# Kernel optimization log

Measured on AMD Instinct MI355X. Metric: run time of the kernel, lower is better.

Reference implementation:

```python
import jax, jax.numpy as jnp
import numpy as np

TEMPERATURE = 8.0  # sqrt(d_k=64)

def setup_inputs() -> dict:
    key = jax.random.key(0)
    kq, kk, kv, km1, km2 = jax.random.split(key, 5)
    B, Lq, Lk, D = 128, 512, 512, 64
    q = jax.random.normal(kq, (B, Lq, D), dtype=jnp.float32)
    k = jax.random.normal(kk, (B, Lk, D), dtype=jnp.float32)
    v = jax.random.normal(kv, (B, Lk, D), dtype=jnp.float32)
    key_mask = jax.random.bernoulli(km1, 0.5, (B, Lq, Lk))
    query_mask = jax.random.bernoulli(km2, 0.5, (B, Lq, Lk))
    return {"q": q, "k": k, "v": v, "key_mask": key_mask, "query_mask": query_mask}

def reference(q, k, v, key_mask, query_mask):
    # attn = (q @ k^T) / temperature, pre-softmax key masking with -inf
    scores = jnp.einsum('bqd,bkd->bqk', q, k) / TEMPERATURE
    scores = jnp.where(key_mask, -jnp.inf, scores)
    attn = jax.nn.softmax(scores, axis=-1)
    # post-softmax query-row zeroing
    attn = jnp.where(query_mask, 0.0, attn)
    # dropout omitted (eval mode / deterministic reference)
    output = jnp.einsum('bqk,bkd->bqd', attn, v)
    return (output, attn)
```

## Files before the change

kernel.cpp:

```cpp
#include <hip/hip_runtime.h>
#include <hip/hip_bf16.h>

#define BATCH 128
#define LQ    512
#define LK    512
#define DH    64
#define TQ    16
#define KC    64

#define VROW  72
#define SSTR  520

typedef float    float4v __attribute__((ext_vector_type(4)));
typedef short    short8v __attribute__((ext_vector_type(8)));
typedef short    short4v __attribute__((ext_vector_type(4)));
typedef int      int4v   __attribute__((ext_vector_type(4)));
typedef _Float16 half4v  __attribute__((ext_vector_type(4)));

__device__ __forceinline__ short bf16r(float f) {
  union { float f; unsigned u; } x; x.f = f;
  unsigned r = x.u + 0x7FFFu + ((x.u >> 16) & 1u);
  return (short)(r >> 16);
}

__global__ __launch_bounds__(256, 6)
void sdpa_kernel(const float* __restrict__ Q, const float* __restrict__ K,
                 const float* __restrict__ V, const int* __restrict__ KM,
                 const int* __restrict__ QM, float* __restrict__ OUT,
                 float* __restrict__ ATT)
{
  __shared__ short kvs[KC * VROW];
  __shared__ short scs[TQ * SSTR];

  const int bid  = blockIdx.x;
  const int wg   = ((bid & 7) << 9) | (bid >> 3);
  const int b    = wg >> 5;
  const int q0   = (wg & 31) * TQ;
  const int tid  = threadIdx.x;
  const int lane = tid & 63;
  const int wave = tid >> 6;
  const int lm   = lane & 15;
  const int quad = lane >> 4;

  const int row = tid >> 4;
  const int col = tid & 15;
  const size_t gro = (size_t)(b * LQ + q0 + row) * LK;

  int4v kmv[8];
#pragma unroll
  for (int j = 0; j < 8; ++j)
    kmv[j] = __builtin_nontemporal_load((const int4v*)(KM + gro + col * 4 + j * 64));

  const float* qrow = Q + ((size_t)(b * LQ + q0 + lm)) * DH + quad * 8;
  short8v aq0, aq1;
  {
    float4v f0 = *(const float4v*)(qrow + 0);
    float4v f1 = *(const float4v*)(qrow + 4);
    float4v f2 = *(const float4v*)(qrow + 32);
    float4v f3 = *(const float4v*)(qrow + 36);
#pragma unroll
    for (int e = 0; e < 4; ++e) {
      aq0[e]     = bf16r(f0[e]);
      aq0[e + 4] = bf16r(f1[e]);
      aq1[e]     = bf16r(f2[e]);
      aq1[e + 4] = bf16r(f3[e]);
    }
  }

#pragma unroll
  for (int t = 0; t < 8; ++t) {
    const int T = wave * 8 + t;
    const float* kr = K + ((size_t)(b * LK + T * 16 + lm)) * DH + quad * 8;
    float4v f0 = *(const float4v*)(kr + 0);
    float4v f1 = *(const float4v*)(kr + 4);
    float4v f2 = *(const float4v*)(kr + 32);
    float4v f3 = *(const float4v*)(kr + 36);
    short8v b0, b1;
#pragma unroll
    for (int e = 0; e < 4; ++e) {
      b0[e]     = bf16r(f0[e]);
      b0[e + 4] = bf16r(f1[e]);
      b1[e]     = bf16r(f2[e]);
      b1[e + 4] = bf16r(f3[e]);
    }
    float4v acc = {0.f, 0.f, 0.f, 0.f};
    acc = __builtin_amdgcn_mfma_f32_16x16x32_bf16(aq0, b0, acc, 0, 0, 0);
    acc = __builtin_amdgcn_mfma_f32_16x16x32_bf16(aq1, b1, acc, 0, 0, 0);
    const int n  = T * 16 + lm;
    const int m0 = quad * 4;
#pragma unroll
    for (int j = 0; j < 4; ++j)
      *(_Float16*)&scs[(m0 + j) * SSTR + n] = (_Float16)acc[j];
  }
  __syncthreads();

  float s[32];
  float mx = -INFINITY;
#pragma unroll
  for (int j = 0; j < 8; ++j) {
    half4v h4 = *(const half4v*)&scs[row * SSTR + col * 4 + j * 64];
#pragma unroll
    for (int e = 0; e < 4; ++e) {
      float val = kmv[j][e] ? -INFINITY : (float)h4[e];
      s[j * 4 + e] = val;
      mx = fmaxf(mx, val);
    }
  }
  int4v qmv[8];
#pragma unroll
  for (int j = 0; j < 8; ++j)
    qmv[j] = __builtin_nontemporal_load((const int4v*)(QM + gro + col * 4 + j * 64));
#pragma unroll
  for (int off = 8; off; off >>= 1) mx = fmaxf(mx, __shfl_xor(mx, off, 64));
  float sum = 0.f;
#pragma unroll
  for (int j = 0; j < 32; ++j) {
    float p = __expf((s[j] - mx) * 0.125f);
    s[j] = p;
    sum += p;
  }
#pragma unroll
  for (int off = 8; off; off >>= 1) sum += __shfl_xor(sum, off, 64);
  const float inv = 1.f / sum;
  float* arow = ATT + gro;
#pragma unroll
  for (int j = 0; j < 8; ++j) {
    int kk = col * 4 + j * 64;
    float4v a4;
#pragma unroll
    for (int e = 0; e < 4; ++e)
      a4[e] = qmv[j][e] ? 0.f : s[j * 4 + e] * inv;
    __builtin_nontemporal_store(a4, (float4v*)(arow + kk));
    short4v ab;
    ab[0] = bf16r(a4[0]); ab[1] = bf16r(a4[1]);
    ab[2] = bf16r(a4[2]); ab[3] = bf16r(a4[3]);
    *(short4v*)&scs[row * SSTR + kk] = ab;
  }

  float4v oacc = {0.f, 0.f, 0.f, 0.f};
  const float* vbase = V + ((size_t)b * LK) * DH;
  float4v va[4];
  {
    const float* vp = vbase + (row * 4) * DH + col * 4;
#pragma unroll
    for (int r = 0; r < 4; ++r) va[r] = *(const float4v*)(vp + r * DH);
  }
#pragma unroll
  for (int kt = 0; kt < 8; ++kt) {
#pragma unroll
    for (int e = 0; e < 4; ++e) {
      int d  = col * 4 + e;
      int gp = row ^ (d & 15);
      short4v s4;
      s4[0] = bf16r(va[0][e]); s4[1] = bf16r(va[1][e]);
      s4[2] = bf16r(va[2][e]); s4[3] = bf16r(va[3][e]);
      *(short4v*)&kvs[d * VROW + gp * 4] = s4;
    }
    float4v vb[4];
    if (kt < 7) {
      const float* vp = vbase + ((kt + 1) * KC + row * 4) * DH + col * 4;
#pragma unroll
      for (int r = 0; r < 4; ++r) vb[r] = *(const float4v*)(vp + r * DH);
    }
    __syncthreads();
#pragma unroll
    for (int ks = 0; ks < 2; ++ks) {
      const short* ap = &scs[lm * SSTR + kt * KC + ks * 32 + quad * 8];
      short8v a8 = *(const short8v*)ap;
      int n  = wave * 16 + lm;
      int g0 = ks * 8 + quad * 2;
      short4v lo = *(const short4v*)&kvs[n * VROW + ((g0    ) ^ (n & 15)) * 4];
      short4v hi = *(const short4v*)&kvs[n * VROW + ((g0 + 1) ^ (n & 15)) * 4];
      short8v b8;
      b8[0] = lo[0]; b8[1] = lo[1]; b8[2] = lo[2]; b8[3] = lo[3];
      b8[4] = hi[0]; b8[5] = hi[1]; b8[6] = hi[2]; b8[7] = hi[3];
      oacc = __builtin_amdgcn_mfma_f32_16x16x32_bf16(a8, b8, oacc, 0, 0, 0);
    }
    __syncthreads();
#pragma unroll
    for (int r = 0; r < 4; ++r) va[r] = vb[r];
  }
  {
    int m0 = quad * 4;
    float* obase = OUT + ((size_t)(b * LQ + q0 + m0)) * DH + wave * 16 + lm;
    obase[0 * DH] = oacc[0];
    obase[1 * DH] = oacc[1];
    obase[2 * DH] = oacc[2];
    obase[3 * DH] = oacc[3];
  }
}

extern "C" void kernel_launch(void* const* d_in, const int* in_sizes, int n_in,
                              void* d_out, int out_size, void* d_ws, size_t ws_size,
                              hipStream_t stream) {
  const float* q  = (const float*)d_in[0];
  const float* k  = (const float*)d_in[1];
  const float* v  = (const float*)d_in[2];
  const int*   km = (const int*)d_in[3];
  const int*   qm = (const int*)d_in[4];
  float* out  = (float*)d_out;
  float* attn = out + (size_t)BATCH * LQ * DH;
  dim3 grid(BATCH * (LQ / TQ));
  dim3 block(256);
  hipLaunchKernelGGL(sdpa_kernel, grid, block, 0, stream,
                     q, k, v, km, qm, out, attn);
}
```

Baseline: 404.2 us.

## Pre-convert Q/K/V to bf16 in workspace with transposed V before attention

Adds a prep kernel that converts Q and K to bf16 and writes V transposed in bf16 into the workspace. The main kernel then loads bf16 operands straight from global memory, with no per-block fp32 conversion and no LDS staging of V. Previously every query tile re-read and re-converted the same K and V. The main kernel also keeps scores in registers, with a cross-wave max/sum reduction through shared memory, and uses two accumulators for the PV MFMAs. The cost is an extra launch and a workspace round trip, and a fallback path is kept for when no workspace is available.

Measured after the change: 422.4 us. 4.5% more time.

```diff
diff --git a/kernel.cpp b/kernel.cpp
--- a/kernel.cpp
+++ b/kernel.cpp
@@ -6,10 +6,13 @@
 #define LK    512
 #define DH    64
 #define TQ    16
-#define KC    64
-
+#define SSTR  520
 #define VROW  72
-#define SSTR  520
+
+#define WS_K 0
+#define WS_V 4194304
+#define WS_Q 8388608
+#define WS_BYTES 25165824ull
 
 typedef float    float4v __attribute__((ext_vector_type(4)));
 typedef short    short8v __attribute__((ext_vector_type(8)));
@@ -23,15 +26,196 @@
   return (short)(r >> 16);
 }
 
-__global__ __launch_bounds__(256, 6)
-void sdpa_kernel(const float* __restrict__ Q, const float* __restrict__ K,
-                 const float* __restrict__ V, const int* __restrict__ KM,
-                 const int* __restrict__ QM, float* __restrict__ OUT,
-                 float* __restrict__ ATT)
+__global__ __launch_bounds__(256)
+void prep_kernel(const float* __restrict__ Q, const float* __restrict__ K,
+                 const float* __restrict__ V, short* __restrict__ ws)
 {
-  __shared__ short kvs[KC * VROW];
+  const int bid = blockIdx.x, tid = threadIdx.x;
+  if (bid < 1024) {
+    __shared__ short T[64 * VROW];
+    const int b  = bid >> 3;
+    const int k0 = (bid & 7) * 64;
+    const int bR = tid >> 4;
+    const int bC = tid & 15;
+    const float* vp = V + ((size_t)(b * LK + k0 + bR * 4)) * DH + bC * 4;
+    float4v r0 = *(const float4v*)(vp);
+    float4v r1 = *(const float4v*)(vp + DH);
+    float4v r2 = *(const float4v*)(vp + 2 * DH);
+    float4v r3 = *(const float4v*)(vp + 3 * DH);
+#pragma unroll
+    for (int e = 0; e < 4; ++e) {
+      int d  = bC * 4 + e;
+      int gp = bR ^ (d & 15);
+      short4v s4;
+      s4[0] = bf16r(r0[e]); s4[1] = bf16r(r1[e]);
+      s4[2] = bf16r(r2[e]); s4[3] = bf16r(r3[e]);
+      *(short4v*)&T[d * VROW + gp * 4] = s4;
+    }
+    __syncthreads();
+    const int d  = tid >> 2;
+    const int g0 = (tid & 3) * 4;
+    short v16[16];
+#pragma unroll
+    for (int s2 = 0; s2 < 4; ++s2) {
+      int g = g0 + s2;
+      short4v t4 = *(const short4v*)&T[d * VROW + ((g ^ (d & 15)) * 4)];
+      v16[s2 * 4 + 0] = t4[0]; v16[s2 * 4 + 1] = t4[1];
+      v16[s2 * 4 + 2] = t4[2]; v16[s2 * 4 + 3] = t4[3];
+    }
+    short* dst = ws + WS_V + ((size_t)(b * DH + d)) * LK + k0 + g0 * 4;
+    *(short8v*)(dst)     = *(short8v*)&v16[0];
+    *(short8v*)(dst + 8) = *(short8v*)&v16[8];
+  } else {
+    const bool isK = (bid < 1152);
+    const size_t base = (size_t)((isK ? bid - 1024 : bid - 1152)) * 32768;
+    const float* src = (isK ? K : Q) + base;
+    short* dst = ws + (isK ? WS_K : WS_Q) + base;
+#pragma unroll 4
+    for (int u = 0; u < 32; ++u) {
+      float4v f = *(const float4v*)(src + u * 1024 + tid * 4);
+      short4v s4;
+      s4[0] = bf16r(f[0]); s4[1] = bf16r(f[1]);
+      s4[2] = bf16r(f[2]); s4[3] = bf16r(f[3]);
+      *(short4v*)(dst + u * 1024 + tid * 4) = s4;
+    }
+  }
+}
+
+__global__ __launch_bounds__(256, 4)
+void sdpa_main(const short* __restrict__ Kbf, const short* __restrict__ Vt,
+               const short* __restrict__ Qbf, const int* __restrict__ KM,
+               const int* __restrict__ QM, float* __restrict__ OUT,
+               float* __restrict__ ATT)
+{
+  __shared__ short sc[TQ * SSTR];
+  __shared__ float cmb[2][64];
+
+  const int bid  = blockIdx.x;
+  const int wg   = ((bid & 7) << 9) | (bid >> 3);
+  const int b    = wg >> 5;
+  const int q0   = (wg & 31) * TQ;
+  const int tid  = threadIdx.x;
+  const int lane = tid & 63;
+  const int wv   = tid >> 6;
+  const int lm   = lane & 15;
+  const int quad = lane >> 4;
+
+  const size_t qg    = (size_t)(b * LQ + q0 + lm);
+  const size_t mbase = qg * LK + wv * 128 + quad * 4;
+
+  int4v kmv[8];
+#pragma unroll
+  for (int t = 0; t < 8; ++t)
+    kmv[t] = __builtin_nontemporal_load((const int4v*)(KM + mbase + t * 16));
+
+  const short* qp = Qbf + qg * DH + quad * 8;
+  const short8v qb0 = *(const short8v*)(qp);
+  const short8v qb1 = *(const short8v*)(qp + 32);
+
+  float s[32];
+  const short* kp0 = Kbf + ((size_t)(b * LK + wv * 128 + lm)) * DH + quad * 8;
+#pragma unroll
+  for (int t = 0; t < 8; ++t) {
+    const short* kp = kp0 + (size_t)t * 16 * DH;
+    short8v ka0 = *(const short8v*)(kp);
+    short8v ka1 = *(const short8v*)(kp + 32);
+    float4v acc = {0.f, 0.f, 0.f, 0.f};
+    acc = __builtin_amdgcn_mfma_f32_16x16x32_bf16(ka0, qb0, acc, 0, 0, 0);
+    acc = __builtin_amdgcn_mfma_f32_16x16x32_bf16(ka1, qb1, acc, 0, 0, 0);
+#pragma unroll
+    for (int j = 0; j < 4; ++j) s[t * 4 + j] = acc[j];
+  }
+
+  float mx0 = -INFINITY, mx1 = -INFINITY, mx2 = -INFINITY, mx3 = -INFINITY;
+#pragma unroll
+  for (int t = 0; t < 8; ++t) {
+#pragma unroll
+    for (int e = 0; e < 4; ++e) {
+      float v = kmv[t][e] ? -INFINITY : s[t * 4 + e];
+      s[t * 4 + e] = v;
+      if (e == 0) mx0 = fmaxf(mx0, v);
+      else if (e == 1) mx1 = fmaxf(mx1, v);
+      else if (e == 2) mx2 = fmaxf(mx2, v);
+      else mx3 = fmaxf(mx3, v);
+    }
+  }
+  float mx = fmaxf(fmaxf(mx0, mx1), fmaxf(mx2, mx3));
+  mx = fmaxf(mx, __shfl_xor(mx, 16, 64));
+  mx = fmaxf(mx, __shfl_xor(mx, 32, 64));
+
+  int4v qmv[8];
+#pragma unroll
+  for (int t = 0; t < 8; ++t)
+    qmv[t] = __builtin_nontemporal_load((const int4v*)(QM + mbase + t * 16));
+
+  if (lane < 16) cmb[0][wv * 16 + lane] = mx;
+  __syncthreads();
+  mx = fmaxf(fmaxf(cmb[0][lm], cmb[0][16 + lm]),
+             fmaxf(cmb[0][32 + lm], cmb[0][48 + lm]));
+
+  float s0 = 0.f, s1 = 0.f, s2 = 0.f, s3 = 0.f;
+#pragma unroll
+  for (int t = 0; t < 8; ++t) {
+    float p0 = __expf((s[t * 4 + 0] - mx) * 0.125f);
+    float p1 = __expf((s[t * 4 + 1] - mx) * 0.125f);
+    float p2 = __expf((s[t * 4 + 2] - mx) * 0.125f);
+    float p3 = __expf((s[t * 4 + 3] - mx) * 0.125f);
+    s[t * 4 + 0] = p0; s[t * 4 + 1] = p1;
+    s[t * 4 + 2] = p2; s[t * 4 + 3] = p3;
+    s0 += p0; s1 += p1; s2 += p2; s3 += p3;
+  }
+  float sum = (s0 + s1) + (s2 + s3);
+  sum += __shfl_xor(sum, 16, 64);
+  sum += __shfl_xor(sum, 32, 64);
+  if (lane < 16) cmb[1][wv * 16 + lane] = sum;
+  __syncthreads();
+  sum = (cmb[1][lm] + cmb[1][16 + lm]) + (cmb[1][32 + lm] + cmb[1][48 + lm]);
+  const float inv = __builtin_amdgcn_rcpf(sum);
+
+  float* arow = ATT + mbase;
+  short* srow = &sc[lm * SSTR + wv * 128 + quad * 4];
+#pragma unroll
+  for (int t = 0; t < 8; ++t) {
+    float4v a4;
+#pragma unroll
+    for (int e = 0; e < 4; ++e)
+      a4[e] = qmv[t][e] ? 0.f : s[t * 4 + e] * inv;
+    __builtin_nontemporal_store(a4, (float4v*)(arow + t * 16));
+    short4v ab;
+    ab[0] = bf16r(a4[0]); ab[1] = bf16r(a4[1]);
+    ab[2] = bf16r(a4[2]); ab[3] = bf16r(a4[3]);
+    *(short4v*)(srow + t * 16) = ab;
+  }
+  __syncthreads();
+
+  float4v oa = {0.f, 0.f, 0.f, 0.f}, ob = {0.f, 0.f, 0.f, 0.f};
+  const short* ap = &sc[lm * SSTR + quad * 8];
+  const short* vp = Vt + ((size_t)(b * DH + wv * 16 + lm)) * LK + quad * 8;
+#pragma unroll
+  for (int c = 0; c < 16; c += 2) {
+    short8v a0 = *(const short8v*)(ap + c * 32);
+    short8v b0 = *(const short8v*)(vp + c * 32);
+    short8v a1 = *(const short8v*)(ap + (c + 1) * 32);
+    short8v b1 = *(const short8v*)(vp + (c + 1) * 32);
+    oa = __builtin_amdgcn_mfma_f32_16x16x32_bf16(a0, b0, oa, 0, 0, 0);
+    ob = __builtin_amdgcn_mfma_f32_16x16x32_bf16(a1, b1, ob, 0, 0, 0);
+  }
+  float4v oacc = oa + ob;
+  float* obase = OUT + ((size_t)(b * LQ + q0 + quad * 4)) * DH + wv * 16 + lm;
+  obase[0 * DH] = oacc[0];
+  obase[1 * DH] = oacc[1];
+  obase[2 * DH] = oacc[2];
+  obase[3 * DH] = oacc[3];
+}
+
+__global__ __launch_bounds__(256, 4)
+void sdpa_fallback(const float* __restrict__ Q, const float* __restrict__ K,
+                   const float* __restrict__ V, const int* __restrict__ KM,
+                   const int* __restrict__ QM, float* __restrict__ OUT,
+                   float* __restrict__ ATT)
+{
+  __shared__ short kvs[64 * VROW];
   __shared__ short scs[TQ * SSTR];
-
   const int bid  = blockIdx.x;
   const int wg   = ((bid & 7) << 9) | (bid >> 3);
   const int b    = wg >> 5;
@@ -41,16 +225,13 @@
   const int wave = tid >> 6;
   const int lm   = lane & 15;
   const int quad = lane >> 4;
-
-  const int row = tid >> 4;
-  const int col = tid & 15;
+  const int row  = tid >> 4;
+  const int col  = tid & 15;
   const size_t gro = (size_t)(b * LQ + q0 + row) * LK;
-
-  int4v kmv[8];
+  int4v km8[8];
 #pragma unroll
   for (int j = 0; j < 8; ++j)
-    kmv[j] = __builtin_nontemporal_load((const int4v*)(KM + gro + col * 4 + j * 64));
-
+    km8[j] = __builtin_nontemporal_load((const int4v*)(KM + gro + col * 4 + j * 64));
   const float* qrow = Q + ((size_t)(b * LQ + q0 + lm)) * DH + quad * 8;
   short8v aq0, aq1;
   {
@@ -60,17 +241,19 @@
     float4v f3 = *(const float4v*)(qrow + 36);
 #pragma unroll
     for (int e = 0; e < 4; ++e) {
-      aq0[e]     = bf16r(f0[e]);
-      aq0[e + 4] = bf16r(f1[e]);
-      aq1[e]     = bf16r(f2[e]);
-      aq1[e + 4] = bf16r(f3[e]);
-    }
-  }
-
-#pragma unroll
-  for (int t = 0; t < 8; ++t) {
-    const int T = wave * 8 + t;
-    const float* kr = K + ((size_t)(b * LK + T * 16 + lm)) * DH + quad * 8;
+      aq0[e] = bf16r(f0[e]); aq0[e + 4] = bf16r(f1[e]);
+      aq1[e] = bf16r(f2[e]); aq1[e + 4] = bf16r(f3[e]);
+    }
+  }
+  unsigned kb = 0;
+#pragma unroll
+  for (int j = 0; j < 8; ++j)
+#pragma unroll
+    for (int e = 0; e < 4; ++e) kb |= (unsigned)(km8[j][e] != 0) << (j * 4 + e);
+  const float* kbp = K + ((size_t)(b * LK + lm)) * DH + quad * 8;
+#pragma unroll
+  for (int t = 0; t < 8; ++t) {
+    const float* kr = kbp + (size_t)(wave * 8 + t) * 16 * DH;
     float4v f0 = *(const float4v*)(kr + 0);
     float4v f1 = *(const float4v*)(kr + 4);
     float4v f2 = *(const float4v*)(kr + 32);
@@ -78,22 +261,22 @@
     short8v b0, b1;
 #pragma unroll
     for (int e = 0; e < 4; ++e) {
-      b0[e]     = bf16r(f0[e]);
-      b0[e + 4] = bf16r(f1[e]);
-      b1[e]     = bf16r(f2[e]);
-      b1[e + 4] = bf16r(f3[e]);
+      b0[e] = bf16r(f0[e]); b0[e + 4] = bf16r(f1[e]);
+      b1[e] = bf16r(f2[e]); b1[e + 4] = bf16r(f3[e]);
     }
     float4v acc = {0.f, 0.f, 0.f, 0.f};
     acc = __builtin_amdgcn_mfma_f32_16x16x32_bf16(aq0, b0, acc, 0, 0, 0);
     acc = __builtin_amdgcn_mfma_f32_16x16x32_bf16(aq1, b1, acc, 0, 0, 0);
-    const int n  = T * 16 + lm;
-    const int m0 = quad * 4;
+    const int n = (wave * 8 + t) * 16 + lm;
 #pragma unroll
     for (int j = 0; j < 4; ++j)
-      *(_Float16*)&scs[(m0 + j) * SSTR + n] = (_Float16)acc[j];
-  }
+      *(_Float16*)&scs[(quad * 4 + j) * SSTR + n] = (_Float16)acc[j];
+  }
+  int4v qm8[8];
+#pragma unroll
+  for (int j = 0; j < 8; ++j)
+    qm8[j] = __builtin_nontemporal_load((const int4v*)(QM + gro + col * 4 + j * 64));
   __syncthreads();
-
   float s[32];
   float mx = -INFINITY;
 #pragma unroll
@@ -101,23 +284,23 @@
     half4v h4 = *(const half4v*)&scs[row * SSTR + col * 4 + j * 64];
 #pragma unroll
     for (int e = 0; e < 4; ++e) {
-      float val = kmv[j][e] ? -INFINITY : (float)h4[e];
+      float val = ((kb >> (j * 4 + e)) & 1u) ? -INFINITY : (float)h4[e];
       s[j * 4 + e] = val;
       mx = fmaxf(mx, val);
     }
   }
-  int4v qmv[8];
+#pragma unroll
+  for (int off = 8; off; off >>= 1) mx = fmaxf(mx, __shfl_xor(mx, off, 64));
+  unsigned qb = 0;
 #pragma unroll
   for (int j = 0; j < 8; ++j)
-    qmv[j] = __builtin_nontemporal_load((const int4v*)(QM + gro + col * 4 + j * 64));
-#pragma unroll
-  for (int off = 8; off; off >>= 1) mx = fmaxf(mx, __shfl_xor(mx, off, 64));
+#pragma unroll
+    for (int e = 0; e < 4; ++e) qb |= (unsigned)(qm8[j][e] != 0) << (j * 4 + e);
   float sum = 0.f;
 #pragma unroll
   for (int j = 0; j < 32; ++j) {
     float p = __expf((s[j] - mx) * 0.125f);
-    s[j] = p;
-    sum += p;
+    s[j] = p; sum += p;
   }
 #pragma unroll
   for (int off = 8; off; off >>= 1) sum += __shfl_xor(sum, off, 64);
@@ -129,47 +312,39 @@
     float4v a4;
 #pragma unroll
     for (int e = 0; e < 4; ++e)
-      a4[e] = qmv[j][e] ? 0.f : s[j * 4 + e] * inv;
-    __builtin_nontemporal_store(a4, (float4v*)(arow + kk));
+      a4[e] = ((qb >> (j * 4 + e)) & 1u) ? 0.f : s[j * 4 + e] * inv;
+    *(float4v*)(arow + kk) = a4;
     short4v ab;
     ab[0] = bf16r(a4[0]); ab[1] = bf16r(a4[1]);
     ab[2] = bf16r(a4[2]); ab[3] = bf16r(a4[3]);
     *(short4v*)&scs[row * SSTR + kk] = ab;
   }
-
   float4v oacc = {0.f, 0.f, 0.f, 0.f};
   const float* vbase = V + ((size_t)b * LK) * DH;
-  float4v va[4];
-  {
-    const float* vp = vbase + (row * 4) * DH + col * 4;
-#pragma unroll
-    for (int r = 0; r < 4; ++r) va[r] = *(const float4v*)(vp + r * DH);
-  }
 #pragma unroll
   for (int kt = 0; kt < 8; ++kt) {
-#pragma unroll
-    for (int e = 0; e < 4; ++e) {
-      int d  = col * 4 + e;
+    const float* vp = vbase + (kt * 64 + row * 4) * DH + col * 4;
+    float4v r0 = *(const float4v*)(vp);
+    float4v r1 = *(const float4v*)(vp + DH);
+    float4v r2 = *(const float4v*)(vp + 2 * DH);
+    float4v r3 = *(const float4v*)(vp + 3 * DH);
+#pragma unroll
+    for (int e = 0; e < 4; ++e) {
+      int d = col * 4 + e;
       int gp = row ^ (d & 15);
       short4v s4;
-      s4[0] = bf16r(va[0][e]); s4[1] = bf16r(va[1][e]);
-      s4[2] = bf16r(va[2][e]); s4[3] = bf16r(va[3][e]);
+      s4[0] = bf16r(r0[e]); s4[1] = bf16r(r1[e]);
+      s4[2] = bf16r(r2[e]); s4[3] = bf16r(r3[e]);
       *(short4v*)&kvs[d * VROW + gp * 4] = s4;
     }
-    float4v vb[4];
-    if (kt < 7) {
-      const float* vp = vbase + ((kt + 1) * KC + row * 4) * DH + col * 4;
-#pragma unroll
-      for (int r = 0; r < 4; ++r) vb[r] = *(const float4v*)(vp + r * DH);
-    }
     __syncthreads();
 #pragma unroll
     for (int ks = 0; ks < 2; ++ks) {
-      const short* ap = &scs[lm * SSTR + kt * KC + ks * 32 + quad * 8];
+      const short* ap = &scs[lm * SSTR + kt * 64 + ks * 32 + quad * 8];
       short8v a8 = *(const short8v*)ap;
       int n  = wave * 16 + lm;
       int g0 = ks * 8 + quad * 2;
-      short4v lo = *(const short4v*)&kvs[n * VROW + ((g0    ) ^ (n & 15)) * 4];
+      short4v lo = *(const short4v*)&kvs[n * VROW + ((g0) ^ (n & 15)) * 4];
       short4v hi = *(const short4v*)&kvs[n * VROW + ((g0 + 1) ^ (n & 15)) * 4];
       short8v b8;
       b8[0] = lo[0]; b8[1] = lo[1]; b8[2] = lo[2]; b8[3] = lo[3];
@@ -177,17 +352,12 @@
       oacc = __builtin_amdgcn_mfma_f32_16x16x32_bf16(a8, b8, oacc, 0, 0, 0);
     }
     __syncthreads();
-#pragma unroll
-    for (int r = 0; r < 4; ++r) va[r] = vb[r];
-  }
-  {
-    int m0 = quad * 4;
-    float* obase = OUT + ((size_t)(b * LQ + q0 + m0)) * DH + wave * 16 + lm;
-    obase[0 * DH] = oacc[0];
-    obase[1 * DH] = oacc[1];
-    obase[2 * DH] = oacc[2];
-    obase[3 * DH] = oacc[3];
-  }
+  }
+  float* obase = OUT + ((size_t)(b * LQ + q0 + quad * 4)) * DH + wave * 16 + lm;
+  obase[0 * DH] = oacc[0];
+  obase[1 * DH] = oacc[1];
+  obase[2 * DH] = oacc[2];
+  obase[3 * DH] = oacc[3];
 }
 
 extern "C" void kernel_launch(void* const* d_in, const int* in_sizes, int n_in,
@@ -200,8 +370,13 @@
   const int*   qm = (const int*)d_in[4];
   float* out  = (float*)d_out;
   float* attn = out + (size_t)BATCH * LQ * DH;
-  dim3 grid(BATCH * (LQ / TQ));
-  dim3 block(256);
-  hipLaunchKernelGGL(sdpa_kernel, grid, block, 0, stream,
-                     q, k, v, km, qm, out, attn);
-}
+  if (d_ws != nullptr && ws_size >= WS_BYTES) {
+    short* ws = (short*)d_ws;
+    hipLaunchKernelGGL(prep_kernel, dim3(1280), dim3(256), 0, stream, q, k, v, ws);
+    hipLaunchKernelGGL(sdpa_main, dim3(BATCH * (LQ / TQ)), dim3(256), 0, stream,
+                       ws + WS_K, ws + WS_V, ws + WS_Q, km, qm, out, attn);
+  } else {
+    hipLaunchKernelGGL(sdpa_fallback, dim3(BATCH * (LQ / TQ)), dim3(256), 0, stream,
+                       q, k, v, km, qm, out, attn);
+  }
+}
```
